# Kernel optimization log

Measured on AMD Instinct MI355X. Metric: run time of the kernel, lower is better.

## Reference

```python
import jax, jax.numpy as jnp
import numpy as np

N = 100_000   # nodes
E = 1_600_000 # edges
G = 128       # graphs in batch
DIN, DOUT = 100, 200


def setup_inputs() -> dict:
    key = jax.random.key(0)
    ks = jax.random.split(key, 12)
    def lin_w(k, fan_in, fan_out):
        return (jax.random.normal(k, (fan_in, fan_out), jnp.float32) / np.sqrt(fan_in)).astype(jnp.float32)
    return {
        "x": jax.random.normal(ks[0], (N, DIN), jnp.float32),
        "edge_index": jax.random.randint(ks[1], (2, E), 0, N, dtype=jnp.int32),
        "batch": jnp.sort(jax.random.randint(ks[2], (N,), 0, G, dtype=jnp.int32)),
        "W1": lin_w(ks[3], DIN, DOUT),  "b1": jnp.zeros((DOUT,), jnp.float32),
        "Wc": lin_w(ks[4], DOUT, DOUT), "bc": jnp.zeros((DOUT,), jnp.float32),
        "W2": lin_w(ks[5], DOUT, DOUT), "b2": jnp.zeros((DOUT,), jnp.float32),
        "W3": lin_w(ks[6], DOUT, DOUT), "b3": jnp.zeros((DOUT,), jnp.float32),
        "Wcls": lin_w(ks[7], DOUT, 2),  "bcls": jnp.zeros((2,), jnp.float32),
    }


def gcn_conv(x, W, b, src, dst, n_nodes):
    """PyG GCNConv: D^{-1/2}(A+I)D^{-1/2} X W + b, symmetric norm with self-loops."""
    h = x @ W  # [N, Dout]
    # degree at targets including the self-loop (+1)
    deg = jax.ops.segment_sum(jnp.ones((src.shape[0],), x.dtype), dst, num_segments=n_nodes) + 1.0
    dinv = jax.lax.rsqrt(deg)  # [N]
    # gather -> normalize -> scatter-add (messages along edges)
    msg = h[src] * (dinv[src] * dinv[dst])[:, None]          # [E, Dout]
    agg = jax.ops.segment_sum(msg, dst, num_segments=n_nodes)  # [N, Dout]
    # self-loop contribution handled analytically: norm_ii = dinv[i]^2
    agg = agg + h * (dinv * dinv)[:, None]
    return agg + b


def reference(x, edge_index, batch, W1, b1, Wc, bc, W2, b2, W3, b3, Wcls, bcls):
    src, dst = edge_index[0], edge_index[1]
    h = jax.nn.relu(gcn_conv(x, W1, b1, src, dst, N))
    # dropout is identity at eval time
    h = h @ Wc + bc
    h = jax.nn.relu(gcn_conv(h, W2, b2, src, dst, N))
    h = gcn_conv(h, W3, b3, src, dst, N)
    pooled = jax.ops.segment_max(h, batch, num_segments=G)  # global max pool -> [G, Dout]
    logits = pooled @ Wcls + bcls
    return jax.nn.softmax(logits, axis=1)
```

## Files before the change

### kernel.cpp

```cpp
#include <hip/hip_runtime.h>
#include <stdint.h>

#define N_NODES 100000
#define N_EDGES 1600000
#define N_GRAPHS 128
#define DIN 100
#define DOUT 200
#define LDH 200
#define LDX 128

#define NB 391
#define BCAP 5120
#define EPB 2048
#define NBLK 782

typedef unsigned short u16;
typedef unsigned int u32;
typedef _Float16 f16;
typedef f16 half8 __attribute__((ext_vector_type(8)));
typedef f16 half4 __attribute__((ext_vector_type(4)));
typedef f16 half2v __attribute__((ext_vector_type(2)));
typedef float floatx4 __attribute__((ext_vector_type(4)));

__device__ __forceinline__ float h2f(u16 h) {
  f16 x; __builtin_memcpy(&x, &h, 2); return (float)x;
}
__device__ __forceinline__ u16 f2h(float f) {
  f16 x = (f16)f; u16 r; __builtin_memcpy(&r, &x, 2); return r;
}
__device__ __forceinline__ u32 encmax(float f) {
  u32 b; __builtin_memcpy(&b, &f, 4);
  return (b & 0x80000000u) ? ~b : (b | 0x80000000u);
}

__device__ __forceinline__ void pack_frag(const float* __restrict__ W, int K, int nfrag,
                                          u16* __restrict__ out, int idx) {
  if (idx >= nfrag) return;
  int lane = idx & 63;
  int t = idx >> 6;
  int ct = t % 13, ks = t / 13;
  int n = ct * 16 + (lane & 15);
  int kbase = ks * 32 + (lane >> 4) * 8;
  u16 v[8];
  #pragma unroll
  for (int j = 0; j < 8; ++j) {
    int k = kbase + j;
    float f = (k < K && n < DOUT) ? W[(size_t)k * DOUT + n] : 0.f;
    v[j] = f2h(f);
  }
  uint4 o;
  o.x = (u32)v[0] | ((u32)v[1] << 16);
  o.y = (u32)v[2] | ((u32)v[3] << 16);
  o.z = (u32)v[4] | ((u32)v[5] << 16);
  o.w = (u32)v[6] | ((u32)v[7] << 16);
  *(uint4*)(out + (size_t)idx * 8) = o;
}

#define B_COMB  158
#define B_PK1   171
#define B_PK3   194
#define B_TOT   (194 + NBLK)
__global__ void k_prep(const int* __restrict__ dst, int* __restrict__ histAll,
                       const float* __restrict__ Wc, const float* __restrict__ bc,
                       const float* __restrict__ W2, float* __restrict__ Wc2,
                       float* __restrict__ bc2, const float* __restrict__ W1,
                       const float* __restrict__ W3, u16* __restrict__ Wpk1,
                       u16* __restrict__ Wpk3) {
  int b = blockIdx.x, t = threadIdx.x;
  if (b < B_COMB) {
    int gid = b * 256 + t;
    if (gid >= 201 * DOUT) return;
    int r = gid / DOUT, c = gid % DOUT;
    const float* a = (r < DOUT) ? (Wc + (size_t)r * DOUT) : bc;
    float s = 0.f;
    for (int k = 0; k < DOUT; ++k) s += a[k] * W2[(size_t)k * DOUT + c];
    if (r < DOUT) Wc2[(size_t)r * DOUT + c] = s;
    else bc2[c] = s;
  } else if (b < B_PK1) {
    pack_frag(W1, DIN, 4 * 13 * 64, Wpk1, (b - B_COMB) * 256 + t);
  } else if (b < B_PK3) {
    pack_frag(W3, DOUT, 7 * 13 * 64, Wpk3, (b - B_PK1) * 256 + t);
  } else {
    __shared__ int hist[NB];
    int hb = b - B_PK3;
    int e0 = hb * EPB;
    int e1 = min(e0 + EPB, N_EDGES);
    for (int j = t; j < NB; j += 256) hist[j] = 0;
    __syncthreads();
    for (int i = e0 + t; i < e1; i += 256)
      atomicAdd(&hist[dst[i] >> 8], 1);
    __syncthreads();
    for (int j = t; j < NB; j += 256)
      histAll[(size_t)hb * NB + j] = hist[j];
  }
}

#define SCAN_TOT (NB + 23)
__global__ void k_scan(const int* __restrict__ histAll, int* __restrict__ baseAll,
                       int* __restrict__ gcur, const float* __restrict__ Wc2,
                       u16* __restrict__ Wpk2) {
  int j = blockIdx.x, t = threadIdx.x;
  if (j >= NB) {
    pack_frag(Wc2, DOUT, 7 * 13 * 64, Wpk2, (j - NB) * 256 + t);
    return;
  }
  __shared__ int s[256];
  int run = 0;
  for (int c = 0; c < NBLK; c += 256) {
    int idx = c + t;
    int v = (idx < NBLK) ? histAll[(size_t)idx * NB + j] : 0;
    s[t] = v;
    __syncthreads();
    for (int o = 1; o < 256; o <<= 1) {
      int x = (t >= o) ? s[t - o] : 0;
      __syncthreads();
      s[t] += x;
      __syncthreads();
    }
    if (idx < NBLK) baseAll[(size_t)idx * NB + j] = run + s[t] - v;
    run += s[255];
    __syncthreads();
  }
  if (t == 0) gcur[j] = run;
}

__global__ void k_scatter(const int* __restrict__ src, const int* __restrict__ dst,
                          const int* __restrict__ baseAll, u32* __restrict__ ebuf) {
  __shared__ int cur[NB];
  int b = blockIdx.x, t = threadIdx.x;
  int e0 = b * EPB;
  int e1 = min(e0 + EPB, N_EDGES);
  for (int j = t; j < NB; j += 256) cur[j] = baseAll[(size_t)b * NB + j];
  __syncthreads();
  for (int i = e0 + t; i < e1; i += 256) {
    int d = dst[i];
    int bk = d >> 8;
    int pos = atomicAdd(&cur[bk], 1);
    if (pos < BCAP)
      ebuf[(size_t)bk * BCAP + pos] = ((u32)src[i] << 8) | (u32)(d & 255);
  }
}

__global__ void k_csr(const u32* __restrict__ ebuf, const int* __restrict__ gcur,
                      int* __restrict__ rowptr, float* __restrict__ dinv,
                      int* __restrict__ colv, const float* __restrict__ x,
                      u16* __restrict__ xs, u32* __restrict__ partenc) {
  __shared__ int s_cnt[256];
  __shared__ int s_cur[256];
  __shared__ int s_scan[256];
  __shared__ int s_g[NB];
  __shared__ int s_red[256];
  __shared__ float s_dinv[256];
  int b = blockIdx.x, t = threadIdx.x;
  int zid = b * 256 + t;
  if (zid < N_GRAPHS * DOUT) partenc[zid] = 0u;
  for (int j = t; j < NB; j += 256) s_g[j] = gcur[j];
  s_cnt[t] = 0;
  __syncthreads();
  int pacc = 0;
  for (int i = t; i < b; i += 256) pacc += s_g[i];
  s_red[t] = pacc;
  __syncthreads();
  for (int o = 128; o > 0; o >>= 1) {
    if (t < o) s_red[t] += s_red[t + o];
    __syncthreads();
  }
  int base = s_red[0];
  if (b == NB - 1 && t == 0) rowptr[N_NODES] = base + s_g[b];
  int cnt = s_g[b];
  int node0 = b << 8;
  const u32* eb = ebuf + (size_t)b * BCAP;
  for (int i = t; i < cnt; i += 256)
    atomicAdd(&s_cnt[eb[i] & 255], 1);
  __syncthreads();
  int v = s_cnt[t];
  s_scan[t] = v;
  __syncthreads();
  for (int o = 1; o < 256; o <<= 1) {
    int x2 = (t >= o) ? s_scan[t - o] : 0;
    __syncthreads();
    s_scan[t] += x2;
    __syncthreads();
  }
  int run = s_scan[t] - v;
  s_cur[t] = base + run;
  float dval = rsqrtf((float)v + 1.0f);
  s_dinv[t] = dval;
  int node = node0 + t;
  if (node < N_NODES) {
    rowptr[node] = base + run;
    dinv[node] = dval;
  }
  __syncthreads();
  for (int i = t; i < cnt; i += 256) {
    u32 e = eb[i];
    int pos = atomicAdd(&s_cur[e & 255], 1);
    colv[pos] = (int)(e >> 8);
  }
  for (int idx = t; idx < 256 * 50; idx += 256) {
    int nl = idx / 50, c = idx % 50;
    int nd = node0 + nl;
    if (nd < N_NODES) {
      float d = s_dinv[nl];
      float2 vv = *(const float2*)(x + (size_t)nd * DIN + c * 2);
      half2v o; o[0] = (f16)(d * vv.x); o[1] = (f16)(d * vv.y);
      *(half2v*)(xs + (size_t)nd * LDX + c * 2) = o;
    }
  }
}

template <int NKS>
__global__ __launch_bounds__(256) void k_gemm_mfma(const u16* __restrict__ A, int lda,
                                                   const u16* __restrict__ Wpk,
                                                   const float* __restrict__ bias,
                                                   const float* __restrict__ rowscale,
                                                   u16* __restrict__ C, int relu, int nrows) {
  int wv = threadIdx.x >> 6;
  int lane = threadIdx.x & 63;
  int r0 = blockIdx.x * 128 + wv * 32;
  int m = lane & 15, q = lane >> 4;
  int row0 = r0 + m, row1 = r0 + 16 + m;
  bool ok0 = (row0 < nrows), ok1 = (row1 < nrows);
  const u16* a0p = A + (size_t)row0 * lda + q * 8;
  const u16* a1p = A + (size_t)row1 * lda + q * 8;

  floatx4 acc0[13], acc1[13];
  #pragma unroll
  for (int ct = 0; ct < 13; ++ct) {
    acc0[ct] = floatx4{0.f, 0.f, 0.f, 0.f};
    acc1[ct] = floatx4{0.f, 0.f, 0.f, 0.f};
  }

  const u16* wp = Wpk + (size_t)lane * 8;
  #pragma unroll
  for (int ks = 0; ks < NKS; ++ks) {
    half8 a0 = ok0 ? *(const half8*)(a0p + ks * 32) : half8{0, 0, 0, 0, 0, 0, 0, 0};
    half8 a1 = ok1 ? *(const half8*)(a1p + ks * 32) : half8{0, 0, 0, 0, 0, 0, 0, 0};
    #pragma unroll
    for (int ct = 0; ct < 13; ++ct) {
      half8 bfr = *(const half8*)(wp + (size_t)(ks * 13 + ct) * 512);
      acc0[ct] = __builtin_amdgcn_mfma_f32_16x16x32_f16(a0, bfr, acc0[ct], 0, 0, 0);
      acc1[ct] = __builtin_amdgcn_mfma_f32_16x16x32_f16(a1, bfr, acc1[ct], 0, 0, 0);
    }
  }

  float sc0[4], sc1[4];
  #pragma unroll
  for (int rg = 0; rg < 4; ++rg) {
    int or0 = r0 + q * 4 + rg;
    int or1 = r0 + 16 + q * 4 + rg;
    sc0[rg] = (rowscale && or0 < nrows) ? rowscale[or0] : 1.f;
    sc1[rg] = (rowscale && or1 < nrows) ? rowscale[or1] : 1.f;
  }

  #pragma unroll
  for (int ct = 0; ct < 13; ++ct) {
    int c = ct * 16 + m;
    if (c >= DOUT) continue;
    float bv = bias ? bias[c] : 0.f;
    #pragma unroll
    for (int rg = 0; rg < 4; ++rg) {
      int or0 = r0 + q * 4 + rg;
      if (or0 < nrows) {
        float v = acc0[ct][rg] + bv;
        if (relu) v = fmaxf(v, 0.f);
        C[(size_t)or0 * LDH + c] = f2h(v * sc0[rg]);
      }
      int or1 = r0 + 16 + q * 4 + rg;
      if (or1 < nrows) {
        float v = acc1[ct][rg] + bv;
        if (relu) v = fmaxf(v, 0.f);
        C[(size_t)or1 * LDH + c] = f2h(v * sc1[rg]);
      }
    }
  }
}

__global__ void k_agg200h(const u16* __restrict__ T, const float* __restrict__ dinv,
                          const int* __restrict__ rowptr, const int* __restrict__ col,
                          const float* __restrict__ bias, u16* __restrict__ OUT,
                          int relu) {
  int wave = (blockIdx.x * blockDim.x + threadIdx.x) >> 6;
  int lane = threadIdx.x & 63;
  if (wave >= N_NODES || lane >= 50) return;
  int node = wave;
  int c4 = lane * 4;
  int beg = __builtin_amdgcn_readfirstlane(rowptr[node]);
  int end = __builtin_amdgcn_readfirstlane(rowptr[node + 1]);
  half4 sv = *(const half4*)(T + (size_t)node * LDH + c4);
  float di = dinv[node];
  float ax = 0.f, ay = 0.f, az = 0.f, aw = 0.f;
  int e = beg;
  for (; e + 16 <= end; e += 16) {
    int s[16];
    half4 tv[16];
    #pragma unroll
    for (int j = 0; j < 16; ++j) s[j] = col[e + j];
    #pragma unroll
    for (int j = 0; j < 16; ++j)
      tv[j] = *(const half4*)(T + (size_t)s[j] * LDH + c4);
    #pragma unroll
    for (int j = 0; j < 16; ++j) {
      ax += (float)tv[j][0]; ay += (float)tv[j][1];
      az += (float)tv[j][2]; aw += (float)tv[j][3];
    }
  }
  if (e + 8 <= end) {
    int s[8];
    half4 tv[8];
    #pragma unroll
    for (int j = 0; j < 8; ++j) s[j] = col[e + j];
    #pragma unroll
    for (int j = 0; j < 8; ++j)
      tv[j] = *(const half4*)(T + (size_t)s[j] * LDH + c4);
    #pragma unroll
    for (int j = 0; j < 8; ++j) {
      ax += (float)tv[j][0]; ay += (float)tv[j][1];
      az += (float)tv[j][2]; aw += (float)tv[j][3];
    }
    e += 8;
  }
  if (e + 4 <= end) {
    int s[4];
    half4 tv[4];
    #pragma unroll
    for (int j = 0; j < 4; ++j) s[j] = col[e + j];
    #pragma unroll
    for (int j = 0; j < 4; ++j)
      tv[j] = *(const half4*)(T + (size_t)s[j] * LDH + c4);
    #pragma unroll
    for (int j = 0; j < 4; ++j) {
      ax += (float)tv[j][0]; ay += (float)tv[j][1];
      az += (float)tv[j][2]; aw += (float)tv[j][3];
    }
    e += 4;
  }
  for (; e < end; ++e) {
    half4 tv = *(const half4*)(T + (size_t)col[e] * LDH + c4);
    ax += (float)tv[0]; ay += (float)tv[1];
    az += (float)tv[2]; aw += (float)tv[3];
  }
  float rx = di * (ax + (float)sv[0]);
  float ry = di * (ay + (float)sv[1]);
  float rz = di * (az + (float)sv[2]);
  float rw = di * (aw + (float)sv[3]);
  if (bias) {
    rx += bias[c4 + 0]; ry += bias[c4 + 1];
    rz += bias[c4 + 2]; rw += bias[c4 + 3];
  }
  if (relu) {
    rx = fmaxf(rx, 0.f); ry = fmaxf(ry, 0.f);
    rz = fmaxf(rz, 0.f); rw = fmaxf(rw, 0.f);
  }
  half4 o;
  o[0] = (f16)rx; o[1] = (f16)ry; o[2] = (f16)rz; o[3] = (f16)rw;
  __builtin_nontemporal_store(o, (half4*)(OUT + (size_t)node * LDH + c4));
}

__global__ void k_agg100h(const u16* __restrict__ T, const float* __restrict__ dinv,
                          const int* __restrict__ rowptr, const int* __restrict__ col,
                          u16* __restrict__ OUT) {
  int wave = (blockIdx.x * blockDim.x + threadIdx.x) >> 6;
  int lane = threadIdx.x & 63;
  if (wave >= N_NODES || lane >= 50) return;
  int node = wave;
  int c2 = lane * 2;
  int beg = __builtin_amdgcn_readfirstlane(rowptr[node]);
  int end = __builtin_amdgcn_readfirstlane(rowptr[node + 1]);
  half2v sv = *(const half2v*)(T + (size_t)node * LDX + c2);
  float di = dinv[node];
  float ax = 0.f, ay = 0.f;
  int e = beg;
  for (; e + 16 <= end; e += 16) {
    int s[16];
    half2v tv[16];
    #pragma unroll
    for (int j = 0; j < 16; ++j) s[j] = col[e + j];
    #pragma unroll
    for (int j = 0; j < 16; ++j)
      tv[j] = *(const half2v*)(T + (size_t)s[j] * LDX + c2);
    #pragma unroll
    for (int j = 0; j < 16; ++j) { ax += (float)tv[j][0]; ay += (float)tv[j][1]; }
  }
  if (e + 8 <= end) {
    int s[8];
    half2v tv[8];
    #pragma unroll
    for (int j = 0; j < 8; ++j) s[j] = col[e + j];
    #pragma unroll
    for (int j = 0; j < 8; ++j)
      tv[j] = *(const half2v*)(T + (size_t)s[j] * LDX + c2);
    #pragma unroll
    for (int j = 0; j < 8; ++j) { ax += (float)tv[j][0]; ay += (float)tv[j][1]; }
    e += 8;
  }
  if (e + 4 <= end) {
    int s[4];
    half2v tv[4];
    #pragma unroll
    for (int j = 0; j < 4; ++j) s[j] = col[e + j];
    #pragma unroll
    for (int j = 0; j < 4; ++j)
      tv[j] = *(const half2v*)(T + (size_t)s[j] * LDX + c2);
    #pragma unroll
    for (int j = 0; j < 4; ++j) { ax += (float)tv[j][0]; ay += (float)tv[j][1]; }
    e += 4;
  }
  for (; e < end; ++e) {
    half2v tv = *(const half2v*)(T + (size_t)col[e] * LDX + c2);
    ax += (float)tv[0]; ay += (float)tv[1];
  }
  half2v o;
  o[0] = (f16)(di * (ax + (float)sv[0]));
  o[1] = (f16)(di * (ay + (float)sv[1]));
  __builtin_nontemporal_store(o, (half2v*)(OUT + (size_t)node * LDX + c2));
}

__global__ void k_aggpool(const u16* __restrict__ T, const float* __restrict__ dinv,
                          const int* __restrict__ rowptr, const int* __restrict__ col,
                          const float* __restrict__ bias, const int* __restrict__ batch,
                          u32* __restrict__ partenc) {
  __shared__ u32 s_enc[4][DOUT];
  int t = threadIdx.x;
  for (int i = t; i < 4 * DOUT; i += 256) ((u32*)s_enc)[i] = 0u;
  __syncthreads();
  int wv = t >> 6, lane = t & 63;
  int nb0 = blockIdx.x * 16;
  int n0 = nb0 + wv * 4;
  int gfirst = batch[nb0];
  int rpl = rowptr[n0 + (lane < 4 ? lane : 4)];
  if (lane < 50) {
    int c4 = lane * 4;
    float b0 = bias[c4 + 0], b1v = bias[c4 + 1], b2v = bias[c4 + 2], b3v = bias[c4 + 3];
    float mx = 0.f, my = 0.f, mz = 0.f, mw = 0.f;
    int curslot = -1;
    for (int i = 0; i < 4; ++i) {
      int node = n0 + i;
      int beg = __builtin_amdgcn_readlane(rpl, i);
      int end = __builtin_amdgcn_readlane(rpl, i + 1);
      half4 sv = *(const half4*)(T + (size_t)node * LDH + c4);
      float di = dinv[node];
      float ax = 0.f, ay = 0.f, az = 0.f, aw = 0.f;
      int e = beg;
      for (; e + 16 <= end; e += 16) {
        int s[16];
        half4 tv[16];
        #pragma unroll
        for (int j = 0; j < 16; ++j) s[j] = col[e + j];
        #pragma unroll
        for (int j = 0; j < 16; ++j)
          tv[j] = *(const half4*)(T + (size_t)s[j] * LDH + c4);
        #pragma unroll
        for (int j = 0; j < 16; ++j) {
          ax += (float)tv[j][0]; ay += (float)tv[j][1];
          az += (float)tv[j][2]; aw += (float)tv[j][3];
        }
      }
      if (e + 8 <= end) {
        int s[8];
        half4 tv[8];
        #pragma unroll
        for (int j = 0; j < 8; ++j) s[j] = col[e + j];
        #pragma unroll
        for (int j = 0; j < 8; ++j)
          tv[j] = *(const half4*)(T + (size_t)s[j] * LDH + c4);
        #pragma unroll
        for (int j = 0; j < 8; ++j) {
          ax += (float)tv[j][0]; ay += (float)tv[j][1];
          az += (float)tv[j][2]; aw += (float)tv[j][3];
        }
        e += 8;
      }
      if (e + 4 <= end) {
        int s[4];
        half4 tv[4];
        #pragma unroll
        for (int j = 0; j < 4; ++j) s[j] = col[e + j];
        #pragma unroll
        for (int j = 0; j < 4; ++j)
          tv[j] = *(const half4*)(T + (size_t)s[j] * LDH + c4);
        #pragma unroll
        for (int j = 0; j < 4; ++j) {
          ax += (float)tv[j][0]; ay += (float)tv[j][1];
          az += (float)tv[j][2]; aw += (float)tv[j][3];
        }
        e += 4;
      }
      for (; e < end; ++e) {
        half4 tv = *(const half4*)(T + (size_t)col[e] * LDH + c4);
        ax += (float)tv[0]; ay += (float)tv[1];
        az += (float)tv[2]; aw += (float)tv[3];
      }
      float rx = di * (ax + (float)sv[0]) + b0;
      float ry = di * (ay + (float)sv[1]) + b1v;
      float rz = di * (az + (float)sv[2]) + b2v;
      float rw = di * (aw + (float)sv[3]) + b3v;
      int slot = batch[node] - gfirst;
      if (slot != curslot) {
        if (curslot >= 0) {
          if (curslot < 4) {
            atomicMax(&s_enc[curslot][c4 + 0], encmax(mx));
            atomicMax(&s_enc[curslot][c4 + 1], encmax(my));
            atomicMax(&s_enc[curslot][c4 + 2], encmax(mz));
            atomicMax(&s_enc[curslot][c4 + 3], encmax(mw));
          } else {
            u32* p = partenc + (size_t)(gfirst + curslot) * DOUT + c4;
            atomicMax(&p[0], encmax(mx)); atomicMax(&p[1], encmax(my));
            atomicMax(&p[2], encmax(mz)); atomicMax(&p[3], encmax(mw));
          }
        }
        curslot = slot;
        mx = rx; my = ry; mz = rz; mw = rw;
      } else {
        mx = fmaxf(mx, rx); my = fmaxf(my, ry);
        mz = fmaxf(mz, rz); mw = fmaxf(mw, rw);
      }
    }
    if (curslot >= 0) {
      if (curslot < 4) {
        atomicMax(&s_enc[curslot][c4 + 0], encmax(mx));
        atomicMax(&s_enc[curslot][c4 + 1], encmax(my));
        atomicMax(&s_enc[curslot][c4 + 2], encmax(mz));
        atomicMax(&s_enc[curslot][c4 + 3], encmax(mw));
      } else {
        u32* p = partenc + (size_t)(gfirst + curslot) * DOUT + c4;
        atomicMax(&p[0], encmax(mx)); atomicMax(&p[1], encmax(my));
        atomicMax(&p[2], encmax(mz)); atomicMax(&p[3], encmax(mw));
      }
    }
  }
  __syncthreads();
  for (int i = t; i < 4 * DOUT; i += 256) {
    u32 v = ((u32*)s_enc)[i];
    if (v) {
      int slot = i / DOUT, d = i % DOUT;
      atomicMax(&partenc[(size_t)(gfirst + slot) * DOUT + d], v);
    }
  }
}

__global__ void k_poolcls(const u32* __restrict__ partenc, const float* __restrict__ Wcls,
                          const float* __restrict__ bcls, float* __restrict__ out) {
  __shared__ float l0s[256], l1s[256];
  int g = blockIdx.x, t = threadIdx.x;
  float c0 = 0.f, c1 = 0.f;
  if (t < DOUT) {
    u32 e = partenc[(size_t)g * DOUT + t];
    float mv;
    if (e == 0u) {
      mv = -3.4e38f;
    } else {
      u32 b = (e & 0x80000000u) ? (e ^ 0x80000000u) : ~e;
      __builtin_memcpy(&mv, &b, 4);
    }
    c0 = mv * Wcls[t * 2 + 0];
    c1 = mv * Wcls[t * 2 + 1];
  }
  l0s[t] = c0; l1s[t] = c1;
  __syncthreads();
  for (int o = 128; o > 0; o >>= 1) {
    if (t < o) { l0s[t] += l0s[t + o]; l1s[t] += l1s[t + o]; }
    __syncthreads();
  }
  if (t == 0) {
    float l0 = l0s[0] + bcls[0], l1 = l1s[0] + bcls[1];
    float m = fmaxf(l0, l1);
    float e0 = expf(l0 - m), e1 = expf(l1 - m);
    float inv = 1.0f / (e0 + e1);
    out[g * 2 + 0] = e0 * inv;
    out[g * 2 + 1] = e1 * inv;
  }
}

static inline size_t align256(size_t x) { return (x + 255) & ~(size_t)255; }

extern "C" void kernel_launch(void* const* d_in, const int* in_sizes, int n_in,
                              void* d_out, int out_size, void* d_ws, size_t ws_size,
                              hipStream_t stream) {
  const float* x     = (const float*)d_in[0];
  const int*   ei    = (const int*)d_in[1];
  const int*   batch = (const int*)d_in[2];
  const float* W1    = (const float*)d_in[3];
  const float* b1    = (const float*)d_in[4];
  const float* Wc    = (const float*)d_in[5];
  const float* bc    = (const float*)d_in[6];
  const float* W2    = (const float*)d_in[7];
  const float* b2    = (const float*)d_in[8];
  const float* W3    = (const float*)d_in[9];
  const float* b3    = (const float*)d_in[10];
  const float* Wcls  = (const float*)d_in[11];
  const float* bcls  = (const float*)d_in[12];
  float* out = (float*)d_out;

  const int N = N_NODES, E = N_EDGES;
  const int* src = ei;
  const int* dst = ei + E;

  char* ws = (char*)d_ws;
  size_t off = 0;
  float* dinv    = (float*)(ws + off); off = align256(off + (size_t)N * 4);
  int*   rowptr  = (int*)  (ws + off); off = align256(off + (size_t)(N + 1) * 4);
  int*   col     = (int*)  (ws + off); off = align256(off + (size_t)E * 4);
  int*   gcur    = (int*)  (ws + off); off = align256(off + (size_t)NB * 4);
  int*   histAll = (int*)  (ws + off); off = align256(off + (size_t)NBLK * NB * 4);
  int*   baseAll = (int*)  (ws + off); off = align256(off + (size_t)NBLK * NB * 4);
  float* Wc2     = (float*)(ws + off); off = align256(off + (size_t)DOUT * DOUT * 4);
  float* bc2     = (float*)(ws + off); off = align256(off + (size_t)DOUT * 4);
  u16*   Wpk1    = (u16*)  (ws + off); off = align256(off + (size_t)4 * 13 * 64 * 8 * 2);
  u16*   Wpk2    = (u16*)  (ws + off); off = align256(off + (size_t)7 * 13 * 64 * 8 * 2);
  u16*   Wpk3    = (u16*)  (ws + off); off = align256(off + (size_t)7 * 13 * 64 * 8 * 2);
  u16*   xs      = (u16*)  (ws + off); off = align256(off + ((size_t)N * LDX + 128) * 2);
  u16*   bufX    = (u16*)  (ws + off); off = align256(off + ((size_t)N * LDX + 128) * 2);
  u16*   buf0    = (u16*)  (ws + off); off = align256(off + ((size_t)N * LDH + 128) * 2);
  u16*   buf1    = (u16*)  (ws + off); off = align256(off + ((size_t)N * LDH + 128) * 2);
  u16*   buf2    = (u16*)  (ws + off); off = align256(off + ((size_t)N * LDH + 128) * 2);

  u32*   ebuf    = (u32*)buf0;
  u32*   partenc = (u32*)histAll;

  k_prep<<<B_TOT, 256, 0, stream>>>(dst, histAll, Wc, bc, W2, Wc2, bc2,
                                    W1, W3, Wpk1, Wpk3);
  k_scan<<<SCAN_TOT, 256, 0, stream>>>(histAll, baseAll, gcur, Wc2, Wpk2);
  k_scatter<<<NBLK, 256, 0, stream>>>(src, dst, baseAll, ebuf);
  k_csr<<<NB, 256, 0, stream>>>(ebuf, gcur, rowptr, dinv, col, x, xs, partenc);

  int gemmb = (N + 127) / 128;
  int aggb  = (N + 3) / 4;
  int aggpb = N / 16;

  k_agg100h<<<aggb, 256, 0, stream>>>(xs, dinv, rowptr, col, bufX);
  k_gemm_mfma<4><<<gemmb, 256, 0, stream>>>(bufX, LDX, Wpk1, b1, nullptr, buf0, 1, N);
  k_gemm_mfma<7><<<gemmb, 256, 0, stream>>>(buf0, LDH, Wpk2, bc2, dinv, buf2, 0, N);
  k_agg200h<<<aggb, 256, 0, stream>>>(buf2, dinv, rowptr, col, b2, buf0, 1);
  k_gemm_mfma<7><<<gemmb, 256, 0, stream>>>(buf0, LDH, Wpk3, nullptr, dinv, buf1, 0, N);
  k_aggpool<<<aggpb, 256, 0, stream>>>(buf1, dinv, rowptr, col, b3, batch, partenc);
  k_poolcls<<<N_GRAPHS, 256, 0, stream>>>(partenc, Wcls, bcls, out);
}
```

Measured before the change: 642.5 us.

## Replace histogram-scan-scatter bucketing with single-pass atomic-reserved scatter

Drops the per-block histogram kernel and the column-wise prefix-scan kernel. Each scatter block now builds a local bucket histogram in shared memory, reserves a contiguous range per bucket with one global atomicAdd on the bucket counter, and writes its edges there, keeping src/dst in registers. This removes two launches and the large histAll/baseAll round trips, but edge order inside a bucket now depends on atomic timing, which makes the CSR column order nondeterministic and so the float summation order can vary between runs.

```diff
diff --git a/kernel.cpp b/kernel.cpp
--- a/kernel.cpp
+++ b/kernel.cpp
@@ -59,8 +59,8 @@
 #define B_COMB  158
 #define B_PK1   171
 #define B_PK3   194
-#define B_TOT   (194 + NBLK)
-__global__ void k_prep(const int* __restrict__ dst, int* __restrict__ histAll,
+#define B_TOT   195
+__global__ void k_prep(int* __restrict__ gcur,
                        const float* __restrict__ Wc, const float* __restrict__ bc,
                        const float* __restrict__ W2, float* __restrict__ Wc2,
                        float* __restrict__ bc2, const float* __restrict__ W1,
@@ -81,63 +81,47 @@
   } else if (b < B_PK3) {
     pack_frag(W3, DOUT, 7 * 13 * 64, Wpk3, (b - B_PK1) * 256 + t);
   } else {
-    __shared__ int hist[NB];
-    int hb = b - B_PK3;
-    int e0 = hb * EPB;
-    int e1 = min(e0 + EPB, N_EDGES);
-    for (int j = t; j < NB; j += 256) hist[j] = 0;
-    __syncthreads();
-    for (int i = e0 + t; i < e1; i += 256)
-      atomicAdd(&hist[dst[i] >> 8], 1);
-    __syncthreads();
-    for (int j = t; j < NB; j += 256)
-      histAll[(size_t)hb * NB + j] = hist[j];
-  }
-}
-
-#define SCAN_TOT (NB + 23)
-__global__ void k_scan(const int* __restrict__ histAll, int* __restrict__ baseAll,
-                       int* __restrict__ gcur, const float* __restrict__ Wc2,
-                       u16* __restrict__ Wpk2) {
-  int j = blockIdx.x, t = threadIdx.x;
-  if (j >= NB) {
-    pack_frag(Wc2, DOUT, 7 * 13 * 64, Wpk2, (j - NB) * 256 + t);
+    for (int j = t; j < NB; j += 256) gcur[j] = 0;
+  }
+}
+
+#define SC_TOT (NBLK + 23)
+__global__ void k_scatter2(const int* __restrict__ src, const int* __restrict__ dst,
+                           int* __restrict__ gcur, u32* __restrict__ ebuf,
+                           const float* __restrict__ Wc2, u16* __restrict__ Wpk2) {
+  int b = blockIdx.x, t = threadIdx.x;
+  if (b >= NBLK) {
+    pack_frag(Wc2, DOUT, 7 * 13 * 64, Wpk2, (b - NBLK) * 256 + t);
     return;
   }
-  __shared__ int s[256];
-  int run = 0;
-  for (int c = 0; c < NBLK; c += 256) {
-    int idx = c + t;
-    int v = (idx < NBLK) ? histAll[(size_t)idx * NB + j] : 0;
-    s[t] = v;
-    __syncthreads();
-    for (int o = 1; o < 256; o <<= 1) {
-      int x = (t >= o) ? s[t - o] : 0;
-      __syncthreads();
-      s[t] += x;
-      __syncthreads();
-    }
-    if (idx < NBLK) baseAll[(size_t)idx * NB + j] = run + s[t] - v;
-    run += s[255];
-    __syncthreads();
-  }
-  if (t == 0) gcur[j] = run;
-}
-
-__global__ void k_scatter(const int* __restrict__ src, const int* __restrict__ dst,
-                          const int* __restrict__ baseAll, u32* __restrict__ ebuf) {
-  __shared__ int cur[NB];
-  int b = blockIdx.x, t = threadIdx.x;
+  __shared__ int hist[NB];
+  __shared__ int gbase[NB];
+  __shared__ int lcur[NB];
   int e0 = b * EPB;
   int e1 = min(e0 + EPB, N_EDGES);
-  for (int j = t; j < NB; j += 256) cur[j] = baseAll[(size_t)b * NB + j];
-  __syncthreads();
-  for (int i = e0 + t; i < e1; i += 256) {
-    int d = dst[i];
-    int bk = d >> 8;
-    int pos = atomicAdd(&cur[bk], 1);
+  for (int j = t; j < NB; j += 256) { hist[j] = 0; lcur[j] = 0; }
+  __syncthreads();
+  int dv[8], sv[8];
+  int nv = 0;
+  #pragma unroll
+  for (int k = 0; k < 8; ++k) {
+    int i = e0 + t + k * 256;
+    if (i < e1) {
+      dv[nv] = dst[i];
+      sv[nv] = src[i];
+      atomicAdd(&hist[dv[nv] >> 8], 1);
+      ++nv;
+    }
+  }
+  __syncthreads();
+  for (int j = t; j < NB; j += 256)
+    if (hist[j] > 0) gbase[j] = atomicAdd(&gcur[j], hist[j]);
+  __syncthreads();
+  for (int k = 0; k < nv; ++k) {
+    int bk = dv[k] >> 8;
+    int pos = gbase[bk] + atomicAdd(&lcur[bk], 1);
     if (pos < BCAP)
-      ebuf[(size_t)bk * BCAP + pos] = ((u32)src[i] << 8) | (u32)(d & 255);
+      ebuf[(size_t)bk * BCAP + pos] = ((u32)sv[k] << 8) | (u32)(dv[k] & 255);
   }
 }
 
@@ -602,8 +586,7 @@
   int*   rowptr  = (int*)  (ws + off); off = align256(off + (size_t)(N + 1) * 4);
   int*   col     = (int*)  (ws + off); off = align256(off + (size_t)E * 4);
   int*   gcur    = (int*)  (ws + off); off = align256(off + (size_t)NB * 4);
-  int*   histAll = (int*)  (ws + off); off = align256(off + (size_t)NBLK * NB * 4);
-  int*   baseAll = (int*)  (ws + off); off = align256(off + (size_t)NBLK * NB * 4);
+  u32*   partenc = (u32*)  (ws + off); off = align256(off + (size_t)N_GRAPHS * DOUT * 4);
   float* Wc2     = (float*)(ws + off); off = align256(off + (size_t)DOUT * DOUT * 4);
   float* bc2     = (float*)(ws + off); off = align256(off + (size_t)DOUT * 4);
   u16*   Wpk1    = (u16*)  (ws + off); off = align256(off + (size_t)4 * 13 * 64 * 8 * 2);
@@ -616,12 +599,9 @@
   u16*   buf2    = (u16*)  (ws + off); off = align256(off + ((size_t)N * LDH + 128) * 2);
 
   u32*   ebuf    = (u32*)buf0;
-  u32*   partenc = (u32*)histAll;
-
-  k_prep<<<B_TOT, 256, 0, stream>>>(dst, histAll, Wc, bc, W2, Wc2, bc2,
-                                    W1, W3, Wpk1, Wpk3);
-  k_scan<<<SCAN_TOT, 256, 0, stream>>>(histAll, baseAll, gcur, Wc2, Wpk2);
-  k_scatter<<<NBLK, 256, 0, stream>>>(src, dst, baseAll, ebuf);
+
+  k_prep<<<B_TOT, 256, 0, stream>>>(gcur, Wc, bc, W2, Wc2, bc2, W1, W3, Wpk1, Wpk3);
+  k_scatter2<<<SC_TOT, 256, 0, stream>>>(src, dst, gcur, ebuf, Wc2, Wpk2);
   k_csr<<<NB, 256, 0, stream>>>(ebuf, gcur, rowptr, dinv, col, x, xs, partenc);
 
   int gemmb = (N + 127) / 128;
```

New measurement: 634.4 us. Within noise of the previous version (-1.3%).
